# Kernel optimization log

Hardware: AMD Instinct MI355X
Metric: run time of the kernel (lower is better)

The kernel has to match this reference:

```python
import jax, jax.numpy as jnp
import numpy as np

S, B, D, H = 2048, 2, 1024, 16
DK = D // H


def _rope_tables(seq_len, dk):
    inv_freq = 1.0 / (10000.0 ** (np.arange(0, dk, 2, dtype=np.float32) / dk))
    ang = np.arange(seq_len, dtype=np.float32)[:, None] * inv_freq[None, :]  # [S, dk/2]
    ang = np.concatenate([ang, ang], axis=-1)  # [S, dk]
    cos = jnp.asarray(np.cos(ang))[None, None]  # [1,1,S,dk]
    sin = jnp.asarray(np.sin(ang))[None, None]
    return cos, sin


def rotate_half(x):
    x1, x2 = x[..., : x.shape[-1] // 2], x[..., x.shape[-1] // 2 :]
    return jnp.concatenate([-x2, x1], axis=-1)


def apply_rope(x, cos, sin):
    return x * cos + rotate_half(x) * sin


def setup_inputs() -> dict:
    key = jax.random.key(0)
    ks = jax.random.split(key, 12)
    Q = jax.random.normal(ks[0], (S, B, D), dtype=jnp.float32)
    K = jax.random.normal(ks[1], (S, B, D), dtype=jnp.float32)
    V = jax.random.normal(ks[2], (S, B, D), dtype=jnp.float32)
    s = 0.02
    W_q = jax.random.normal(ks[3], (D, D), dtype=jnp.float32) * s
    W_k = jax.random.normal(ks[4], (D, D), dtype=jnp.float32) * s
    W_v = jax.random.normal(ks[5], (D, D), dtype=jnp.float32) * s
    W_o = jax.random.normal(ks[6], (D, D), dtype=jnp.float32) * s
    b_q = jnp.zeros((D,), jnp.float32)
    b_k = jnp.zeros((D,), jnp.float32)
    b_v = jnp.zeros((D,), jnp.float32)
    b_o = jnp.zeros((D,), jnp.float32)
    cos, sin = _rope_tables(S, DK)
    mask = jnp.triu(jnp.ones((S, S), dtype=bool), k=1)[None, None]  # causal, True = masked
    return {
        "Q": Q, "K": K, "V": V,
        "W_q": W_q, "b_q": b_q, "W_k": W_k, "b_k": b_k,
        "W_v": W_v, "b_v": b_v, "W_o": W_o, "b_o": b_o,
        "q_rotary_cos": cos, "q_rotary_sin": sin,
        "k_rotary_cos": cos, "k_rotary_sin": sin,
        "mask": mask,
    }


def reference(Q, K, V, W_q, b_q, W_k, b_k, W_v, b_v, W_o, b_o,
              q_rotary_cos, q_rotary_sin, k_rotary_cos, k_rotary_sin, mask):
    q_len, bsz, _ = Q.shape
    # [S,B,D] -> [S,B,H,dk] -> [B,H,S,dk]
    def proj(x, W, b):
        y = x @ W.T + b
        return y.reshape(x.shape[0], bsz, H, DK).transpose(1, 2, 0, 3)
    q_s = apply_rope(proj(Q, W_q, b_q), q_rotary_cos, q_rotary_sin)
    k_s = apply_rope(proj(K, W_k, b_k), k_rotary_cos, k_rotary_sin)
    v_s = proj(V, W_v, b_v)
    scores = jnp.einsum("bhqd,bhkd->bhqk", q_s, k_s) / jnp.sqrt(jnp.float32(DK))
    scores = jnp.where(mask, jnp.float32(-1e9), scores)
    attn = jax.nn.softmax(scores, axis=-1)
    context = jnp.einsum("bhqk,bhkd->bhqd", attn, v_s)  # [B,H,S,dk]
    context = context.transpose(2, 0, 1, 3).reshape(q_len, bsz, D)
    return context @ W_o.T + b_o
```

## Files before the change

kernel.cpp:

```cpp
#include <hip/hip_runtime.h>
#include <cstdint>
#include <cstddef>

typedef __bf16 bf16;
typedef __bf16 bf16x2 __attribute__((ext_vector_type(2)));
typedef __bf16 bf16x4 __attribute__((ext_vector_type(4)));
typedef __bf16 bf16x8 __attribute__((ext_vector_type(8)));
typedef float f32x4 __attribute__((ext_vector_type(4)));

#define S_LEN 2048
#define BATCH 2
#define DM 1024
#define NH 16
#define DKH 64
#define MTOT (S_LEN * BATCH)

__device__ __forceinline__ void gload_lds16(const void* g, void* l) {
    __builtin_amdgcn_global_load_lds((const __attribute__((address_space(1))) uint32_t*)g,
                                     (__attribute__((address_space(3))) uint32_t*)l, 16, 0, 0);
}

__device__ __forceinline__ uint32_t pack2(float a, float b) {
    bf16x2 v; v[0] = (bf16)a; v[1] = (bf16)b;
    return __builtin_bit_cast(uint32_t, v);
}

struct ConvArgs { const float* src[7]; bf16* dst[7]; };

__global__ __launch_bounds__(256) void convert_all(ConvArgs a) {
    int gid = blockIdx.x * 256 + threadIdx.x;
    int tid, off;
    if (gid < 3 * 524288) { tid = gid >> 19; off = gid & 524287; }
    else { int r = gid - 3 * 524288; tid = 3 + (r >> 17); off = r & 131071; }
    const float4* s4 = (const float4*)a.src[tid];
    float4 x = s4[2 * off], y = s4[2 * off + 1];
    bf16x8 v;
    v[0] = (bf16)x.x; v[1] = (bf16)x.y; v[2] = (bf16)x.z; v[3] = (bf16)x.w;
    v[4] = (bf16)y.x; v[5] = (bf16)y.y; v[6] = (bf16)y.z; v[7] = (bf16)y.w;
    *(bf16x8*)(a.dst[tid] + 8 * (size_t)off) = v;
}

__device__ __forceinline__ void gemm_core(const bf16* __restrict__ A, const bf16* __restrict__ Bt,
                                          const float* __restrict__ bias, void* __restrict__ out,
                                          int mode, const float* __restrict__ cosp,
                                          const float* __restrict__ sinp, bf16* As, bf16* Bs) {
    const int K = DM;
    int t = threadIdx.x;
    int lane = t & 63, wave = t >> 6;
    int lm = lane & 15, quad = lane >> 4;
    int m0 = blockIdx.y * 128, n0 = blockIdx.x * 128;
    int wm = (wave >> 1) * 64, wn = (wave & 1) * 64;
    f32x4 acc[4][4] = {};
    int g0 = t, g1 = t + 256;
    const bf16* agp0 = A + (size_t)(m0 + (g0 >> 2)) * K + (g0 & 3) * 8;
    const bf16* agp1 = A + (size_t)(m0 + (g1 >> 2)) * K + (g1 & 3) * 8;
    const bf16* bgp0 = Bt + (size_t)(n0 + (g0 >> 2)) * K + (g0 & 3) * 8;
    const bf16* bgp1 = Bt + (size_t)(n0 + (g1 >> 2)) * K + (g1 & 3) * 8;
    bf16* al0 = As + wave * 512;
    bf16* al1 = As + 2048 + wave * 512;
    bf16* bl0 = Bs + wave * 512;
    bf16* bl1 = Bs + 2048 + wave * 512;
    for (int k0 = 0; k0 < K; k0 += 32) {
        gload_lds16(agp0 + k0, al0);
        gload_lds16(agp1 + k0, al1);
        gload_lds16(bgp0 + k0, bl0);
        gload_lds16(bgp1 + k0, bl1);
        __syncthreads();
        bf16x8 af[4], bfr[4];
#pragma unroll
        for (int i = 0; i < 4; ++i)
            af[i] = *(const bf16x8*)(As + (wm + i * 16 + lm) * 32 + quad * 8);
#pragma unroll
        for (int j = 0; j < 4; ++j)
            bfr[j] = *(const bf16x8*)(Bs + (wn + j * 16 + lm) * 32 + quad * 8);
#pragma unroll
        for (int i = 0; i < 4; ++i)
#pragma unroll
            for (int j = 0; j < 4; ++j)
                acc[i][j] = __builtin_amdgcn_mfma_f32_16x16x32_bf16(af[i], bfr[j], acc[i][j], 0, 0, 0);
        __syncthreads();
    }
#pragma unroll
    for (int j = 0; j < 4; ++j) {
        float bcol = bias[n0 + wn + j * 16 + lm];
#pragma unroll
        for (int i = 0; i < 4; ++i)
#pragma unroll
            for (int r = 0; r < 4; ++r) acc[i][j][r] += bcol;
    }
#pragma unroll
    for (int i = 0; i < 4; ++i) {
#pragma unroll
        for (int j = 0; j < 4; ++j) {
            int col = n0 + wn + j * 16 + lm;
#pragma unroll
            for (int r = 0; r < 4; ++r) {
                int row = m0 + wm + i * 16 + quad * 4 + r;
                float val = acc[i][j][r];
                if (mode == 1) {
                    int s = row >> 1, b = row & 1;
                    int h = col >> 6, dk = col & 63;
                    ((bf16*)out)[((size_t)(b * NH + h) * DKH + dk) * S_LEN + s] = (bf16)val;
                } else if (mode == 2) {
                    ((float*)out)[(size_t)row * DM + col] = val;
                } else {
                    int s = row >> 1, dk = col & 63;
                    float c = cosp[s * 64 + dk], sn = sinp[s * 64 + dk];
                    float partner = acc[i][j ^ 2][r];
                    float v2 = val * c + (dk < 32 ? -partner : partner) * sn;
                    if (mode == 3) v2 *= 0.125f * 1.44269504088896f;
                    ((bf16*)out)[(size_t)row * DM + col] = (bf16)v2;
                }
            }
        }
    }
}

struct QKVArgs {
    const bf16* A[3]; const bf16* W[3]; const float* bias[3];
    void* out[3]; const float* cs[3]; const float* sn[3]; int mode[3];
};

__global__ __launch_bounds__(256) void gemm_qkv(QKVArgs args) {
    __shared__ __align__(16) bf16 As[128 * 32];
    __shared__ __align__(16) bf16 Bs[128 * 32];
    int z = blockIdx.z;
    gemm_core(args.A[z], args.W[z], args.bias[z], args.out[z], args.mode[z],
              args.cs[z], args.sn[z], As, Bs);
}

__global__ __launch_bounds__(256) void gemm_one(const bf16* __restrict__ A, const bf16* __restrict__ Bt,
                                                const float* __restrict__ bias, void* __restrict__ out) {
    __shared__ __align__(16) bf16 As[128 * 32];
    __shared__ __align__(16) bf16 Bs[128 * 32];
    gemm_core(A, Bt, bias, out, 2, nullptr, nullptr, As, Bs);
}

#define LROW 72
#define LBUF (64 * LROW)

__global__ __launch_bounds__(256, 3) void flash_kernel(const bf16* __restrict__ qp, const bf16* __restrict__ kp,
                                                       const bf16* __restrict__ vT, bf16* __restrict__ ctx) {
    int qt = 31 - blockIdx.x;
    int bh = blockIdx.y;
    int b = bh >> 4, h = bh & 15;
    int t = threadIdx.x, lane = t & 63, wave = t >> 6;
    int lm = lane & 15, quad = lane >> 4;
    __shared__ __align__(16) bf16 Ks[2 * LBUF];
    __shared__ __align__(16) bf16 Vs[2 * LBUF];
    __shared__ __align__(16) uint32_t Pb[4][16 * 36];
    uint32_t* pw = &Pb[wave][0];
    const int q0w = qt * 64 + wave * 16;
    const size_t kstep = (size_t)BATCH * DM;

    const bf16* qrow = qp + ((size_t)(q0w + lm) * BATCH + b) * DM + h * DKH;
    bf16x8 aq0 = *(const bf16x8*)(qrow + quad * 8);
    bf16x8 aq1 = *(const bf16x8*)(qrow + 32 + quad * 8);
    f32x4 o[4] = {};
    float m_i = -1e30f, l_i = 0.f;

    int g0 = t, g1 = t + 256;
    int r0 = g0 >> 3, c0 = g0 & 7, r1 = g1 >> 3, c1 = g1 & 7;
    const bf16* kg0 = kp + ((size_t)r0 * BATCH + b) * DM + h * DKH + c0 * 8;
    const bf16* kg1 = kp + ((size_t)r1 * BATCH + b) * DM + h * DKH + c1 * 8;
    const bf16* vg0 = vT + ((size_t)(bh * DKH + r0)) * S_LEN + c0 * 8;
    const bf16* vg1 = vT + ((size_t)(bh * DKH + r1)) * S_LEN + c1 * 8;
    int lo0 = r0 * LROW + c0 * 8;
    int lo1 = r1 * LROW + c1 * 8;

    const int niter = qt + 1;
    {
        bf16x8 ka = *(const bf16x8*)kg0;
        bf16x8 kb2 = *(const bf16x8*)kg1;
        bf16x8 va = *(const bf16x8*)vg0;
        bf16x8 vb2 = *(const bf16x8*)vg1;
        *(bf16x8*)(Ks + lo0) = ka;
        *(bf16x8*)(Ks + lo1) = kb2;
        *(bf16x8*)(Vs + lo0) = va;
        *(bf16x8*)(Vs + lo1) = vb2;
    }
    __syncthreads();

    for (int it = 0; it < niter; ++it) {
        int kv0 = it << 6;
        int cb = it & 1, nb = cb ^ 1;
        bool hn = (it + 1) < niter;
        bf16x8 ka, kb2, va, vb2;
        if (hn) {
            size_t koff = (size_t)(kv0 + 64) * kstep;
            ka  = *(const bf16x8*)(kg0 + koff);
            kb2 = *(const bf16x8*)(kg1 + koff);
            va  = *(const bf16x8*)(vg0 + kv0 + 64);
            vb2 = *(const bf16x8*)(vg1 + kv0 + 64);
        }
        if (kv0 <= q0w + 15) {
            const bf16* Kb = Ks + cb * LBUF;
            const bf16* Vb = Vs + cb * LBUF;
            const f32x4 zero = {0.f, 0.f, 0.f, 0.f};
            f32x4 sc[4];
#pragma unroll
            for (int nt = 0; nt < 4; ++nt) {
                bf16x8 kf0 = *(const bf16x8*)(Kb + (nt * 16 + lm) * LROW + quad * 8);
                bf16x8 kf1 = *(const bf16x8*)(Kb + (nt * 16 + lm) * LROW + 32 + quad * 8);
                sc[nt] = __builtin_amdgcn_mfma_f32_16x16x32_bf16(kf0, aq0, zero, 0, 0, 0);
                sc[nt] = __builtin_amdgcn_mfma_f32_16x16x32_bf16(kf1, aq1, sc[nt], 0, 0, 0);
            }
            if (kv0 + 63 > q0w) {
#pragma unroll
                for (int nt = 0; nt < 4; ++nt)
#pragma unroll
                    for (int r = 0; r < 4; ++r) {
                        int kvg = kv0 + nt * 16 + quad * 4 + r;
                        if (kvg > q0w + lm) sc[nt][r] = -1e30f;
                    }
            }
            float mx = sc[0][0];
#pragma unroll
            for (int nt = 0; nt < 4; ++nt)
#pragma unroll
                for (int r = 0; r < 4; ++r) mx = fmaxf(mx, sc[nt][r]);
            mx = fmaxf(mx, __shfl_xor(mx, 16, 64));
            mx = fmaxf(mx, __shfl_xor(mx, 32, 64));
            float mn = fmaxf(m_i, mx);
            float al = exp2f(m_i - mn);
            m_i = mn;
            float rs = 0.f;
            uint32_t pk[8];
#pragma unroll
            for (int nt = 0; nt < 4; ++nt)
#pragma unroll
                for (int rp = 0; rp < 2; ++rp) {
                    float p0 = exp2f(sc[nt][2 * rp] - mn);
                    float p1 = exp2f(sc[nt][2 * rp + 1] - mn);
                    rs += p0 + p1;
                    pk[nt * 2 + rp] = pack2(p0, p1);
                }
            rs += __shfl_xor(rs, 16, 64);
            rs += __shfl_xor(rs, 32, 64);
            l_i = l_i * al + rs;
#pragma unroll
            for (int dt = 0; dt < 4; ++dt) o[dt] *= al;
#pragma unroll
            for (int nt = 0; nt < 4; ++nt)
#pragma unroll
                for (int rp = 0; rp < 2; ++rp)
                    pw[lm * 36 + nt * 8 + quad * 2 + rp] = pk[nt * 2 + rp];
            __builtin_amdgcn_wave_barrier();
            const uint32_t* pr = pw + lm * 36;
            bf16x8 pf0 = *(const bf16x8*)(pr + quad * 4);
            bf16x8 pf1 = *(const bf16x8*)(pr + 16 + quad * 4);
#pragma unroll
            for (int dt = 0; dt < 4; ++dt) {
                bf16x8 vf0 = *(const bf16x8*)(Vb + (dt * 16 + lm) * LROW + quad * 8);
                bf16x8 vf1 = *(const bf16x8*)(Vb + (dt * 16 + lm) * LROW + 32 + quad * 8);
                o[dt] = __builtin_amdgcn_mfma_f32_16x16x32_bf16(vf0, pf0, o[dt], 0, 0, 0);
                o[dt] = __builtin_amdgcn_mfma_f32_16x16x32_bf16(vf1, pf1, o[dt], 0, 0, 0);
            }
            __builtin_amdgcn_wave_barrier();
        }
        if (hn) {
            bf16* Kn = Ks + nb * LBUF;
            bf16* Vn = Vs + nb * LBUF;
            *(bf16x8*)(Kn + lo0) = ka;
            *(bf16x8*)(Kn + lo1) = kb2;
            *(bf16x8*)(Vn + lo0) = va;
            *(bf16x8*)(Vn + lo1) = vb2;
        }
        __syncthreads();
    }
    float linv = 1.f / l_i;
    int qg = q0w + lm;
    bf16* crow = ctx + ((size_t)qg * BATCH + b) * DM + h * DKH;
#pragma unroll
    for (int dt = 0; dt < 4; ++dt) {
        bf16x4 v;
#pragma unroll
        for (int r = 0; r < 4; ++r) v[r] = (bf16)(o[dt][r] * linv);
        *(bf16x4*)(crow + dt * 16 + quad * 4) = v;
    }
}

extern "C" void kernel_launch(void* const* d_in, const int* in_sizes, int n_in,
                              void* d_out, int out_size, void* d_ws, size_t ws_size,
                              hipStream_t stream) {
    const float* Q    = (const float*)d_in[0];
    const float* K    = (const float*)d_in[1];
    const float* V    = (const float*)d_in[2];
    const float* Wq   = (const float*)d_in[3];
    const float* bq   = (const float*)d_in[4];
    const float* Wk   = (const float*)d_in[5];
    const float* bk   = (const float*)d_in[6];
    const float* Wv   = (const float*)d_in[7];
    const float* bv   = (const float*)d_in[8];
    const float* Wo   = (const float*)d_in[9];
    const float* bo   = (const float*)d_in[10];
    const float* qcos = (const float*)d_in[11];
    const float* qsin = (const float*)d_in[12];
    const float* kcos = (const float*)d_in[13];
    const float* ksin = (const float*)d_in[14];

    char* ws = (char*)d_ws;
    const size_t SZ_ACT = (size_t)MTOT * DM * sizeof(bf16);
    const size_t SZ_W   = (size_t)DM * DM * sizeof(bf16);
    bf16* qb  = (bf16*)ws; ws += SZ_ACT;
    bf16* kb  = (bf16*)ws; ws += SZ_ACT;
    bf16* vb  = (bf16*)ws; ws += SZ_ACT;
    bf16* wqb = (bf16*)ws; ws += SZ_W;
    bf16* wkb = (bf16*)ws; ws += SZ_W;
    bf16* wvb = (bf16*)ws; ws += SZ_W;
    bf16* wob = (bf16*)ws; ws += SZ_W;
    bf16* qpr = (bf16*)ws; ws += SZ_ACT;
    bf16* kpr = (bf16*)ws; ws += SZ_ACT;
    bf16* vTp = (bf16*)ws; ws += SZ_ACT;
    bf16* ctx = (bf16*)ws; ws += SZ_ACT;

    ConvArgs ca;
    ca.src[0] = Q;  ca.dst[0] = qb;
    ca.src[1] = K;  ca.dst[1] = kb;
    ca.src[2] = V;  ca.dst[2] = vb;
    ca.src[3] = Wq; ca.dst[3] = wqb;
    ca.src[4] = Wk; ca.dst[4] = wkb;
    ca.src[5] = Wv; ca.dst[5] = wvb;
    ca.src[6] = Wo; ca.dst[6] = wob;
    convert_all<<<8192, 256, 0, stream>>>(ca);

    QKVArgs qa;
    qa.A[0] = qb; qa.W[0] = wqb; qa.bias[0] = bq; qa.out[0] = qpr; qa.mode[0] = 3; qa.cs[0] = qcos; qa.sn[0] = qsin;
    qa.A[1] = kb; qa.W[1] = wkb; qa.bias[1] = bk; qa.out[1] = kpr; qa.mode[1] = 4; qa.cs[1] = kcos; qa.sn[1] = ksin;
    qa.A[2] = vb; qa.W[2] = wvb; qa.bias[2] = bv; qa.out[2] = vTp; qa.mode[2] = 1; qa.cs[2] = nullptr; qa.sn[2] = nullptr;
    gemm_qkv<<<dim3(DM / 128, MTOT / 128, 3), 256, 0, stream>>>(qa);

    flash_kernel<<<dim3(32, BATCH * NH), 256, 0, stream>>>(qpr, kpr, vTp, ctx);

    gemm_one<<<dim3(DM / 128, MTOT / 128), 256, 0, stream>>>(ctx, wob, bo, (float*)d_out);
}
```

Baseline: 309.9 us.

## Shrink GEMM N-tile to 64 and single-buffer swizzled LDS in flash attention

The projection GEMMs move from 128x128 to 128x64 output tiles. Each wave now computes a 32x64 slice, which doubles the grid and fills more CUs, at the cost of less operand reuse per block. The flash kernel drops its padded double-buffered K/V LDS tiles in favour of single 64x64 buffers with an XOR swizzle to avoid bank conflicts, and raises launch_bounds occupancy from 3 to 4. The single buffer needs an extra __syncthreads per iteration before the next tile is written, which reduces overlap between loads and compute.

```diff
diff --git a/kernel.cpp b/kernel.cpp
--- a/kernel.cpp
+++ b/kernel.cpp
@@ -48,33 +48,29 @@
     int t = threadIdx.x;
     int lane = t & 63, wave = t >> 6;
     int lm = lane & 15, quad = lane >> 4;
-    int m0 = blockIdx.y * 128, n0 = blockIdx.x * 128;
-    int wm = (wave >> 1) * 64, wn = (wave & 1) * 64;
-    f32x4 acc[4][4] = {};
-    int g0 = t, g1 = t + 256;
-    const bf16* agp0 = A + (size_t)(m0 + (g0 >> 2)) * K + (g0 & 3) * 8;
-    const bf16* agp1 = A + (size_t)(m0 + (g1 >> 2)) * K + (g1 & 3) * 8;
-    const bf16* bgp0 = Bt + (size_t)(n0 + (g0 >> 2)) * K + (g0 & 3) * 8;
-    const bf16* bgp1 = Bt + (size_t)(n0 + (g1 >> 2)) * K + (g1 & 3) * 8;
+    int m0 = blockIdx.y * 128, n0 = blockIdx.x * 64;
+    int wm = wave * 32;
+    f32x4 acc[2][4] = {};
+    const bf16* agp0 = A + (size_t)(m0 + (t >> 2)) * K + (t & 3) * 8;
+    const bf16* agp1 = A + (size_t)(m0 + 64 + (t >> 2)) * K + (t & 3) * 8;
+    const bf16* bgp0 = Bt + (size_t)(n0 + (t >> 2)) * K + (t & 3) * 8;
     bf16* al0 = As + wave * 512;
     bf16* al1 = As + 2048 + wave * 512;
     bf16* bl0 = Bs + wave * 512;
-    bf16* bl1 = Bs + 2048 + wave * 512;
     for (int k0 = 0; k0 < K; k0 += 32) {
         gload_lds16(agp0 + k0, al0);
         gload_lds16(agp1 + k0, al1);
         gload_lds16(bgp0 + k0, bl0);
-        gload_lds16(bgp1 + k0, bl1);
         __syncthreads();
-        bf16x8 af[4], bfr[4];
-#pragma unroll
-        for (int i = 0; i < 4; ++i)
+        bf16x8 af[2], bfr[4];
+#pragma unroll
+        for (int i = 0; i < 2; ++i)
             af[i] = *(const bf16x8*)(As + (wm + i * 16 + lm) * 32 + quad * 8);
 #pragma unroll
         for (int j = 0; j < 4; ++j)
-            bfr[j] = *(const bf16x8*)(Bs + (wn + j * 16 + lm) * 32 + quad * 8);
-#pragma unroll
-        for (int i = 0; i < 4; ++i)
+            bfr[j] = *(const bf16x8*)(Bs + (j * 16 + lm) * 32 + quad * 8);
+#pragma unroll
+        for (int i = 0; i < 2; ++i)
 #pragma unroll
             for (int j = 0; j < 4; ++j)
                 acc[i][j] = __builtin_amdgcn_mfma_f32_16x16x32_bf16(af[i], bfr[j], acc[i][j], 0, 0, 0);
@@ -82,17 +78,17 @@
     }
 #pragma unroll
     for (int j = 0; j < 4; ++j) {
-        float bcol = bias[n0 + wn + j * 16 + lm];
-#pragma unroll
-        for (int i = 0; i < 4; ++i)
+        float bcol = bias[n0 + j * 16 + lm];
+#pragma unroll
+        for (int i = 0; i < 2; ++i)
 #pragma unroll
             for (int r = 0; r < 4; ++r) acc[i][j][r] += bcol;
     }
 #pragma unroll
-    for (int i = 0; i < 4; ++i) {
+    for (int i = 0; i < 2; ++i) {
 #pragma unroll
         for (int j = 0; j < 4; ++j) {
-            int col = n0 + wn + j * 16 + lm;
+            int col = n0 + j * 16 + lm;
 #pragma unroll
             for (int r = 0; r < 4; ++r) {
                 int row = m0 + wm + i * 16 + quad * 4 + r;
@@ -123,7 +119,7 @@
 
 __global__ __launch_bounds__(256) void gemm_qkv(QKVArgs args) {
     __shared__ __align__(16) bf16 As[128 * 32];
-    __shared__ __align__(16) bf16 Bs[128 * 32];
+    __shared__ __align__(16) bf16 Bs[64 * 32];
     int z = blockIdx.z;
     gemm_core(args.A[z], args.W[z], args.bias[z], args.out[z], args.mode[z],
               args.cs[z], args.sn[z], As, Bs);
@@ -132,26 +128,22 @@
 __global__ __launch_bounds__(256) void gemm_one(const bf16* __restrict__ A, const bf16* __restrict__ Bt,
                                                 const float* __restrict__ bias, void* __restrict__ out) {
     __shared__ __align__(16) bf16 As[128 * 32];
-    __shared__ __align__(16) bf16 Bs[128 * 32];
+    __shared__ __align__(16) bf16 Bs[64 * 32];
     gemm_core(A, Bt, bias, out, 2, nullptr, nullptr, As, Bs);
 }
 
-#define LROW 72
-#define LBUF (64 * LROW)
-
-__global__ __launch_bounds__(256, 3) void flash_kernel(const bf16* __restrict__ qp, const bf16* __restrict__ kp,
+__global__ __launch_bounds__(256, 4) void flash_kernel(const bf16* __restrict__ qp, const bf16* __restrict__ kp,
                                                        const bf16* __restrict__ vT, bf16* __restrict__ ctx) {
     int qt = 31 - blockIdx.x;
     int bh = blockIdx.y;
     int b = bh >> 4, h = bh & 15;
     int t = threadIdx.x, lane = t & 63, wave = t >> 6;
     int lm = lane & 15, quad = lane >> 4;
-    __shared__ __align__(16) bf16 Ks[2 * LBUF];
-    __shared__ __align__(16) bf16 Vs[2 * LBUF];
+    __shared__ __align__(16) bf16 Ks[64 * 64];
+    __shared__ __align__(16) bf16 Vs[64 * 64];
     __shared__ __align__(16) uint32_t Pb[4][16 * 36];
     uint32_t* pw = &Pb[wave][0];
     const int q0w = qt * 64 + wave * 16;
-    const size_t kstep = (size_t)BATCH * DM;
 
     const bf16* qrow = qp + ((size_t)(q0w + lm) * BATCH + b) * DM + h * DKH;
     bf16x8 aq0 = *(const bf16x8*)(qrow + quad * 8);
@@ -159,49 +151,45 @@
     f32x4 o[4] = {};
     float m_i = -1e30f, l_i = 0.f;
 
-    int g0 = t, g1 = t + 256;
-    int r0 = g0 >> 3, c0 = g0 & 7, r1 = g1 >> 3, c1 = g1 & 7;
+    int r0 = t >> 3, c0 = t & 7;
+    int r1 = r0 + 32;
     const bf16* kg0 = kp + ((size_t)r0 * BATCH + b) * DM + h * DKH + c0 * 8;
-    const bf16* kg1 = kp + ((size_t)r1 * BATCH + b) * DM + h * DKH + c1 * 8;
+    const bf16* kg1 = kp + ((size_t)r1 * BATCH + b) * DM + h * DKH + c0 * 8;
     const bf16* vg0 = vT + ((size_t)(bh * DKH + r0)) * S_LEN + c0 * 8;
-    const bf16* vg1 = vT + ((size_t)(bh * DKH + r1)) * S_LEN + c1 * 8;
-    int lo0 = r0 * LROW + c0 * 8;
-    int lo1 = r1 * LROW + c1 * 8;
+    const bf16* vg1 = vT + ((size_t)(bh * DKH + r1)) * S_LEN + c0 * 8;
+    int lk0 = r0 * 64 + (c0 ^ (r0 & 7)) * 8;
+    int lk1 = r1 * 64 + (c0 ^ (r1 & 7)) * 8;
+    const size_t kstep = (size_t)64 * BATCH * DM;
 
     const int niter = qt + 1;
-    {
-        bf16x8 ka = *(const bf16x8*)kg0;
-        bf16x8 kb2 = *(const bf16x8*)kg1;
-        bf16x8 va = *(const bf16x8*)vg0;
-        bf16x8 vb2 = *(const bf16x8*)vg1;
-        *(bf16x8*)(Ks + lo0) = ka;
-        *(bf16x8*)(Ks + lo1) = kb2;
-        *(bf16x8*)(Vs + lo0) = va;
-        *(bf16x8*)(Vs + lo1) = vb2;
-    }
+    bf16x8 ka = *(const bf16x8*)kg0;
+    bf16x8 kb2 = *(const bf16x8*)kg1;
+    bf16x8 va = *(const bf16x8*)vg0;
+    bf16x8 vb2 = *(const bf16x8*)vg1;
+    *(bf16x8*)(Ks + lk0) = ka;
+    *(bf16x8*)(Ks + lk1) = kb2;
+    *(bf16x8*)(Vs + lk0) = va;
+    *(bf16x8*)(Vs + lk1) = vb2;
     __syncthreads();
 
     for (int it = 0; it < niter; ++it) {
         int kv0 = it << 6;
-        int cb = it & 1, nb = cb ^ 1;
         bool hn = (it + 1) < niter;
-        bf16x8 ka, kb2, va, vb2;
         if (hn) {
-            size_t koff = (size_t)(kv0 + 64) * kstep;
+            size_t koff = (size_t)(it + 1) * kstep;
             ka  = *(const bf16x8*)(kg0 + koff);
             kb2 = *(const bf16x8*)(kg1 + koff);
-            va  = *(const bf16x8*)(vg0 + kv0 + 64);
-            vb2 = *(const bf16x8*)(vg1 + kv0 + 64);
+            va  = *(const bf16x8*)(vg0 + (it + 1) * 64);
+            vb2 = *(const bf16x8*)(vg1 + (it + 1) * 64);
         }
         if (kv0 <= q0w + 15) {
-            const bf16* Kb = Ks + cb * LBUF;
-            const bf16* Vb = Vs + cb * LBUF;
             const f32x4 zero = {0.f, 0.f, 0.f, 0.f};
             f32x4 sc[4];
 #pragma unroll
             for (int nt = 0; nt < 4; ++nt) {
-                bf16x8 kf0 = *(const bf16x8*)(Kb + (nt * 16 + lm) * LROW + quad * 8);
-                bf16x8 kf1 = *(const bf16x8*)(Kb + (nt * 16 + lm) * LROW + 32 + quad * 8);
+                int krow = nt * 16 + lm;
+                bf16x8 kf0 = *(const bf16x8*)(Ks + krow * 64 + ((quad ^ (krow & 7)) * 8));
+                bf16x8 kf1 = *(const bf16x8*)(Ks + krow * 64 + (((quad + 4) ^ (krow & 7)) * 8));
                 sc[nt] = __builtin_amdgcn_mfma_f32_16x16x32_bf16(kf0, aq0, zero, 0, 0, 0);
                 sc[nt] = __builtin_amdgcn_mfma_f32_16x16x32_bf16(kf1, aq1, sc[nt], 0, 0, 0);
             }
@@ -251,20 +239,20 @@
             bf16x8 pf1 = *(const bf16x8*)(pr + 16 + quad * 4);
 #pragma unroll
             for (int dt = 0; dt < 4; ++dt) {
-                bf16x8 vf0 = *(const bf16x8*)(Vb + (dt * 16 + lm) * LROW + quad * 8);
-                bf16x8 vf1 = *(const bf16x8*)(Vb + (dt * 16 + lm) * LROW + 32 + quad * 8);
+                int vrow = dt * 16 + lm;
+                bf16x8 vf0 = *(const bf16x8*)(Vs + vrow * 64 + ((quad ^ (vrow & 7)) * 8));
+                bf16x8 vf1 = *(const bf16x8*)(Vs + vrow * 64 + (((quad + 4) ^ (vrow & 7)) * 8));
                 o[dt] = __builtin_amdgcn_mfma_f32_16x16x32_bf16(vf0, pf0, o[dt], 0, 0, 0);
                 o[dt] = __builtin_amdgcn_mfma_f32_16x16x32_bf16(vf1, pf1, o[dt], 0, 0, 0);
             }
             __builtin_amdgcn_wave_barrier();
         }
+        __syncthreads();
         if (hn) {
-            bf16* Kn = Ks + nb * LBUF;
-            bf16* Vn = Vs + nb * LBUF;
-            *(bf16x8*)(Kn + lo0) = ka;
-            *(bf16x8*)(Kn + lo1) = kb2;
-            *(bf16x8*)(Vn + lo0) = va;
-            *(bf16x8*)(Vn + lo1) = vb2;
+            *(bf16x8*)(Ks + lk0) = ka;
+            *(bf16x8*)(Ks + lk1) = kb2;
+            *(bf16x8*)(Vs + lk0) = va;
+            *(bf16x8*)(Vs + lk1) = vb2;
         }
         __syncthreads();
     }
@@ -328,9 +316,9 @@
     qa.A[0] = qb; qa.W[0] = wqb; qa.bias[0] = bq; qa.out[0] = qpr; qa.mode[0] = 3; qa.cs[0] = qcos; qa.sn[0] = qsin;
     qa.A[1] = kb; qa.W[1] = wkb; qa.bias[1] = bk; qa.out[1] = kpr; qa.mode[1] = 4; qa.cs[1] = kcos; qa.sn[1] = ksin;
     qa.A[2] = vb; qa.W[2] = wvb; qa.bias[2] = bv; qa.out[2] = vTp; qa.mode[2] = 1; qa.cs[2] = nullptr; qa.sn[2] = nullptr;
-    gemm_qkv<<<dim3(DM / 128, MTOT / 128, 3), 256, 0, stream>>>(qa);
+    gemm_qkv<<<dim3(DM / 64, MTOT / 128, 3), 256, 0, stream>>>(qa);
 
     flash_kernel<<<dim3(32, BATCH * NH), 256, 0, stream>>>(qpr, kpr, vTp, ctx);
 
-    gemm_one<<<dim3(DM / 128, MTOT / 128), 256, 0, stream>>>(ctx, wob, bo, (float*)d_out);
-}
+    gemm_one<<<dim3(DM / 64, MTOT / 128), 256, 0, stream>>>(ctx, wob, bo, (float*)d_out);
+}
```

Measured after the change: 301.1 us. 1.03x faster.
